# Optimization experiments

Hardware: AMD Instinct MI355X
Metric: run time of the kernel (lower is better)

## Reference

```python
import jax, jax.numpy as jnp
import numpy as np
from jax import lax

EPS = 1e-5

def conv2d(x, w):
    # x: [B,C,H,W], w: [O,I,kh,kw], VALID, stride 1
    return lax.conv_general_dilated(x, w, (1, 1), 'VALID',
                                    dimension_numbers=('NCHW', 'OIHW', 'NCHW'))

def bn_eval(x, g, b, m, v):
    # per-channel eval-mode batchnorm on NCHW
    scale = g / jnp.sqrt(v + EPS)
    return x * scale[None, :, None, None] + (b - m * scale)[None, :, None, None]

def xcorr_depthwise(search, kernel):
    # search: [B,C,Hs,Ws], kernel: [B,C,hk,wk] -> [B,C,Ho,Wo]
    B, C, Hs, Ws = search.shape
    hk, wk = kernel.shape[2], kernel.shape[3]
    s = search.reshape(1, B * C, Hs, Ws)
    k = kernel.reshape(B * C, 1, hk, wk)
    out = lax.conv_general_dilated(s, k, (1, 1), 'VALID',
                                   dimension_numbers=('NCHW', 'OIHW', 'NCHW'),
                                   feature_group_count=B * C)
    return out.reshape(B, C, out.shape[2], out.shape[3])

def setup_inputs() -> dict:
    key = jax.random.key(0)
    ks = jax.random.split(key, 16)
    B, C, HID, OUT = 64, 256, 256, 10
    d = {}
    d['kernel'] = jax.random.normal(ks[0], (B, C, 7, 7), jnp.float32)
    d['search'] = jax.random.normal(ks[1], (B, C, 31, 31), jnp.float32)
    # conv_kernel branch
    d['ck_w'] = jax.random.normal(ks[2], (HID, C, 3, 3), jnp.float32) * 0.02
    d['ck_g'] = jnp.ones((HID,), jnp.float32)
    d['ck_b'] = jnp.zeros((HID,), jnp.float32)
    d['ck_m'] = jax.random.normal(ks[3], (HID,), jnp.float32) * 0.1
    d['ck_v'] = jax.random.uniform(ks[4], (HID,), jnp.float32, 0.5, 1.5)
    # conv_search branch
    d['cs_w'] = jax.random.normal(ks[5], (HID, C, 3, 3), jnp.float32) * 0.02
    d['cs_g'] = jnp.ones((HID,), jnp.float32)
    d['cs_b'] = jnp.zeros((HID,), jnp.float32)
    d['cs_m'] = jax.random.normal(ks[6], (HID,), jnp.float32) * 0.1
    d['cs_v'] = jax.random.uniform(ks[7], (HID,), jnp.float32, 0.5, 1.5)
    # head: 1x1 conv (no bias) + BN + ReLU + 1x1 conv (bias)
    d['h1_w'] = jax.random.normal(ks[8], (HID, HID), jnp.float32) * 0.05
    d['h_g'] = jnp.ones((HID,), jnp.float32)
    d['h_b'] = jnp.zeros((HID,), jnp.float32)
    d['h_m'] = jax.random.normal(ks[9], (HID,), jnp.float32) * 0.1
    d['h_v'] = jax.random.uniform(ks[10], (HID,), jnp.float32, 0.5, 1.5)
    d['h2_w'] = jax.random.normal(ks[11], (OUT, HID), jnp.float32) * 0.05
    d['h2_b'] = jnp.zeros((OUT,), jnp.float32)
    return d

def reference(kernel, search, ck_w, ck_g, ck_b, ck_m, ck_v,
              cs_w, cs_g, cs_b, cs_m, cs_v,
              h1_w, h_g, h_b, h_m, h_v, h2_w, h2_b):
    k = jax.nn.relu(bn_eval(conv2d(kernel, ck_w), ck_g, ck_b, ck_m, ck_v))   # [B,256,5,5]
    s = jax.nn.relu(bn_eval(conv2d(search, cs_w), cs_g, cs_b, cs_m, cs_v))   # [B,256,29,29]
    feat = xcorr_depthwise(s, k)                                             # [B,256,25,25]
    x = jnp.einsum('oi,bihw->bohw', h1_w, feat)
    x = jax.nn.relu(bn_eval(x, h_g, h_b, h_m, h_v))
    out = jnp.einsum('oi,bihw->bohw', h2_w, x) + h2_b[None, :, None, None]   # [B,10,25,25]
    return out
```

## Files before the change

kernel.cpp:

```cpp
#include <hip/hip_runtime.h>
#include <cstddef>
#include <cstdint>

#define BN_EPS 1e-5f

typedef __attribute__((ext_vector_type(8))) __bf16 bf16x8;
typedef __attribute__((ext_vector_type(4))) float f32x4;

__device__ inline unsigned short f2bf(float f) {
    unsigned u = __builtin_bit_cast(unsigned, f);
    unsigned r = (u + 0x7fff + ((u >> 16) & 1)) >> 16;
    return (unsigned short)r;
}
__device__ inline float bf2f(unsigned short u) {
    return __builtin_bit_cast(float, (unsigned)u << 16);
}

#define GLDS16(g, l)                                                        \
    __builtin_amdgcn_global_load_lds(                                       \
        (const __attribute__((address_space(1))) void*)(g),                 \
        (__attribute__((address_space(3))) void*)(l), 16, 0, 0)

template<int H, int W, int WP>
__device__ inline void nhwc_body(int bh, const float* __restrict__ in,
                                 unsigned short* __restrict__ out)
{
    __shared__ unsigned short tl[256][WP];
    const int tid = threadIdx.x;
    const int b = bh / H, h = bh - b * H;
    const int g = tid >> 5, wl = tid & 31;
    const float* base = in + (size_t)b * 256 * (H * W) + (size_t)h * W;
    if (wl < W) {
        #pragma unroll
        for (int cc = 0; cc < 32; ++cc) {
            const int c = cc * 8 + g;
            tl[c][wl] = f2bf(base[(size_t)c * (H * W) + wl]);
        }
    }
    __syncthreads();
    unsigned short* dst = out + (size_t)bh * W * 256 + tid;
    #pragma unroll
    for (int w = 0; w < W; ++w) dst[w * 256] = tl[tid][w];
}

__global__ __launch_bounds__(256)
void prep_kernel(const float* __restrict__ srch, const float* __restrict__ kin,
                 const float* __restrict__ cs_w, const float* __restrict__ ck_w,
                 const float* __restrict__ h1_w, const float* __restrict__ h2_w,
                 unsigned short* __restrict__ s16, unsigned short* __restrict__ k16,
                 unsigned short* __restrict__ wTs, unsigned short* __restrict__ wTk,
                 unsigned short* __restrict__ h1w16, unsigned short* __restrict__ h2w16,
                 int G31, int G7)
{
    const int bid = blockIdx.x;
    if (bid < G31) {
        nhwc_body<31, 31, 33>(bid, srch, s16);
    } else if (bid < G31 + G7) {
        nhwc_body<7, 7, 9>(bid - G31, kin, k16);
    } else {
        const int i = (bid - G31 - G7) * 256 + threadIdx.x;
        if (i < 589824) {
            const int ic = i & 255, t = i >> 8, oc = t & 255, khkw = t >> 8;
            wTs[i] = f2bf(cs_w[(size_t)((oc << 8) + ic) * 9 + khkw]);
        } else if (i < 1179648) {
            const int j = i - 589824;
            const int ic = j & 255, t = j >> 8, oc = t & 255, khkw = t >> 8;
            wTk[j] = f2bf(ck_w[(size_t)((oc << 8) + ic) * 9 + khkw]);
        } else if (i < 1245184) {
            const int j = i - 1179648;
            h1w16[j] = f2bf(h1_w[j]);
        } else if (i < 1249280) {
            const int j = i - 1245184;
            const int oc = j >> 8, ic = j & 255;
            h2w16[j] = (oc < 10) ? f2bf(h2_w[oc * 256 + ic]) : (unsigned short)0;
        }
    }
}

struct ConvParams {
    const unsigned short* bsrc;
    const unsigned short* wT;
    const float *bg, *bb, *bm, *bv;
    unsigned short* out;
    int IH, IW, OW, PPB, N;
};

__global__ __launch_bounds__(256)
void conv3x3_kernel(ConvParams S, ConvParams K, int Gs)
{
    __shared__ __align__(16) unsigned short Alds[128 * 64];
    __shared__ __align__(16) unsigned short Blds[128 * 64];

    const int tid  = threadIdx.x;
    const int lane = tid & 63;
    const int wid  = tid >> 6;

    const int raw = blockIdx.x;
    ConvParams P;
    int tileid;
    if (raw < Gs) {
        P = S;
        const int q8 = Gs >> 3, r8 = Gs & 7;
        const int xcd = raw & 7, seq = raw >> 3;
        tileid = (xcd < r8 ? xcd * (q8 + 1) : r8 * (q8 + 1) + (xcd - r8) * q8) + seq;
    } else {
        P = K;
        tileid = raw - Gs;
    }
    const int pt  = tileid >> 1;
    const int oct = tileid & 1;
    const int oc0 = oct << 7;
    const int p0  = pt << 7;

    int aoff[4], brow[4], bgs8[4], ldsrow[4];
    #pragma unroll
    for (int i = 0; i < 4; ++i) {
        const int r  = i * 32 + wid * 8 + (lane >> 3);
        const int gs = (lane & 7) ^ (r & 7);
        aoff[i] = (oc0 + r) * 256 + gs * 8;
        int pg = p0 + r; if (pg > P.N - 1) pg = P.N - 1;
        const int bb_ = pg / P.PPB;
        const int p   = pg - bb_ * P.PPB;
        const int oh  = p / P.OW, ow = p - oh * P.OW;
        brow[i] = (bb_ * P.IH + oh) * P.IW + ow;
        bgs8[i] = gs * 8;
        ldsrow[i] = (i * 32 + wid * 8) * 64;
    }

    const int q_  = lane >> 4;
    const int lr  = lane & 15;
    const int wm0 = (wid >> 1) * 64;
    const int wn0 = (wid & 1) * 64;
    const int g0  = q_ ^ (lane & 7);
    const int g1  = (4 + q_) ^ (lane & 7);
    const unsigned short* Abase = &Alds[(wm0 + lr) * 64];
    const unsigned short* Bbase = &Blds[(wn0 + lr) * 64];

    f32x4 acc[4][4] = {};

    int kh = 0, kw = 0;
    for (int khkw = 0; khkw < 9; ++khkw) {
        const size_t wslice = (size_t)khkw << 16;
        const int tapadd = kh * P.IW + kw;
        for (int ics = 0; ics < 4; ++ics) {
            const int ic0 = ics * 64;
            __syncthreads();
            #pragma unroll
            for (int i = 0; i < 4; ++i) {
                GLDS16(P.wT + wslice + aoff[i] + ic0, &Alds[ldsrow[i]]);
                GLDS16(P.bsrc + (size_t)(brow[i] + tapadd) * 256 + ic0 + bgs8[i],
                       &Blds[ldsrow[i]]);
            }
            __syncthreads();

            bf16x8 bfr[4][2];
            #pragma unroll
            for (int n = 0; n < 4; ++n) {
                bfr[n][0] = *(const bf16x8*)(Bbase + n * 1024 + g0 * 8);
                bfr[n][1] = *(const bf16x8*)(Bbase + n * 1024 + g1 * 8);
            }
            #pragma unroll
            for (int m = 0; m < 4; ++m) {
                bf16x8 a0 = *(const bf16x8*)(Abase + m * 1024 + g0 * 8);
                bf16x8 a1 = *(const bf16x8*)(Abase + m * 1024 + g1 * 8);
                #pragma unroll
                for (int n = 0; n < 4; ++n) {
                    acc[m][n] = __builtin_amdgcn_mfma_f32_16x16x32_bf16(
                                    a0, bfr[n][0], acc[m][n], 0, 0, 0);
                    acc[m][n] = __builtin_amdgcn_mfma_f32_16x16x32_bf16(
                                    a1, bfr[n][1], acc[m][n], 0, 0, 0);
                }
            }
        }
        if (++kw == 3) { kw = 0; ++kh; }
    }

    #pragma unroll
    for (int m = 0; m < 4; ++m) {
        const int ocm = oc0 + wm0 + m * 16 + q_ * 4;
        float sc[4], sh[4];
        #pragma unroll
        for (int r = 0; r < 4; ++r) {
            sc[r] = P.bg[ocm + r] * rsqrtf(P.bv[ocm + r] + BN_EPS);
            sh[r] = P.bb[ocm + r] - P.bm[ocm + r] * sc[r];
        }
        #pragma unroll
        for (int n = 0; n < 4; ++n) {
            const int pg = p0 + wn0 + n * 16 + lr;
            if (pg < P.N) {
                unsigned e0 = f2bf(fmaxf(acc[m][n][0] * sc[0] + sh[0], 0.f));
                unsigned e1 = f2bf(fmaxf(acc[m][n][1] * sc[1] + sh[1], 0.f));
                unsigned e2 = f2bf(fmaxf(acc[m][n][2] * sc[2] + sh[2], 0.f));
                unsigned e3 = f2bf(fmaxf(acc[m][n][3] * sc[3] + sh[3], 0.f));
                uint2 v; v.x = e0 | (e1 << 16); v.y = e2 | (e3 << 16);
                *(uint2*)(P.out + (size_t)pg * 256 + ocm) = v;
            }
        }
    }
}

__global__ __launch_bounds__(256)
void xcorr_nhwc_kernel(const unsigned short* __restrict__ sfeat,
                       const unsigned short* __restrict__ kfeat,
                       unsigned short* __restrict__ xc2)
{
    const int bid = blockIdx.x;
    const int b = bid / 25, oh = bid - b * 25;
    const int c = threadIdx.x;

    float kv[25];
    const unsigned short* kp = kfeat + (size_t)b * 25 * 256 + c;
    #pragma unroll
    for (int t = 0; t < 25; ++t) kv[t] = bf2f(kp[t * 256]);

    float acc[25];
    #pragma unroll
    for (int ow = 0; ow < 25; ++ow) acc[ow] = 0.f;

    const unsigned short* sp = sfeat + ((size_t)(b * 29 + oh)) * 29 * 256 + c;
    #pragma unroll
    for (int i = 0; i < 5; ++i) {
        #pragma unroll
        for (int w = 0; w < 29; ++w) {
            const float sv = bf2f(sp[(i * 29 + w) * 256]);
            #pragma unroll
            for (int j = 0; j < 5; ++j) {
                if (j <= w && w - j <= 24)
                    acc[w - j] += sv * kv[i * 5 + j];
            }
        }
    }

    unsigned short* op = xc2 + ((size_t)(b * 625 + oh * 25)) * 256 + c;
    #pragma unroll
    for (int ow = 0; ow < 25; ++ow) op[ow * 256] = f2bf(acc[ow]);
}

__global__ __launch_bounds__(256)
void fused_head_kernel(const unsigned short* __restrict__ xc2,
                       const unsigned short* __restrict__ h1w16,
                       const unsigned short* __restrict__ h2w16,
                       const float* __restrict__ bn_g,
                       const float* __restrict__ bn_b,
                       const float* __restrict__ bn_m,
                       const float* __restrict__ bn_v,
                       const float* __restrict__ h2b,
                       float* __restrict__ out)
{
    __shared__ __align__(16) unsigned short lds[20480];
    unsigned short* Alds = lds;
    unsigned short* Blds = lds + 16384;
    unsigned short* Ylds = lds;

    const int tid  = threadIdx.x;
    const int lane = tid & 63;
    const int wid  = tid >> 6;
    const int p0   = blockIdx.x * 64;

    const int lrow = lane >> 3;
    const int gs   = 0;
    (void)gs;

    int aoffs[8], aldsr[8];
    #pragma unroll
    for (int s = 0; s < 8; ++s) {
        const int rowb = s * 32 + wid * 8;
        const int row  = rowb + lrow;
        const int g    = (lane & 7) ^ (row & 7);
        aoffs[s] = row * 256 + g * 8;
        aldsr[s] = rowb * 64;
    }
    int boffs[2], bldsr[2];
    #pragma unroll
    for (int t = 0; t < 2; ++t) {
        const int rowb = t * 32 + wid * 8;
        const int row  = rowb + lrow;
        const int g    = (lane & 7) ^ (row & 7);
        boffs[t] = (p0 + row) * 256 + g * 8;
        bldsr[t] = rowb * 64;
    }

    const int q_ = lane >> 4;
    const int lr = lane & 15;
    const int wm = wid >> 1;
    const int wn = wid & 1;
    const int g0 = q_ ^ (lane & 7);
    const int g1 = (4 + q_) ^ (lane & 7);
    const unsigned short* Abase = &Alds[(wm * 128 + lr) * 64];
    const unsigned short* Bbase = &Blds[(wn * 32 + lr) * 64];

    f32x4 acc[8][2] = {};

    for (int ics = 0; ics < 4; ++ics) {
        const int ic0 = ics * 64;
        __syncthreads();
        #pragma unroll
        for (int s = 0; s < 8; ++s)
            GLDS16(h1w16 + aoffs[s] + ic0, &Alds[aldsr[s]]);
        #pragma unroll
        for (int t = 0; t < 2; ++t)
            GLDS16(xc2 + boffs[t] + ic0, &Blds[bldsr[t]]);
        __syncthreads();

        bf16x8 bfr[2][2];
        #pragma unroll
        for (int n = 0; n < 2; ++n) {
            bfr[n][0] = *(const bf16x8*)(Bbase + n * 1024 + g0 * 8);
            bfr[n][1] = *(const bf16x8*)(Bbase + n * 1024 + g1 * 8);
        }
        #pragma unroll
        for (int m = 0; m < 8; ++m) {
            bf16x8 a0 = *(const bf16x8*)(Abase + m * 1024 + g0 * 8);
            bf16x8 a1 = *(const bf16x8*)(Abase + m * 1024 + g1 * 8);
            #pragma unroll
            for (int n = 0; n < 2; ++n) {
                acc[m][n] = __builtin_amdgcn_mfma_f32_16x16x32_bf16(
                                a0, bfr[n][0], acc[m][n], 0, 0, 0);
                acc[m][n] = __builtin_amdgcn_mfma_f32_16x16x32_bf16(
                                a1, bfr[n][1], acc[m][n], 0, 0, 0);
            }
        }
    }

    __syncthreads();
    #pragma unroll
    for (int m = 0; m < 8; ++m) {
        const int ocm = wm * 128 + m * 16 + q_ * 4;
        float sc[4], sh[4];
        #pragma unroll
        for (int r = 0; r < 4; ++r) {
            sc[r] = bn_g[ocm + r] * rsqrtf(bn_v[ocm + r] + BN_EPS);
            sh[r] = bn_b[ocm + r] - bn_m[ocm + r] * sc[r];
        }
        #pragma unroll
        for (int n = 0; n < 2; ++n) {
            const int pl = wn * 32 + n * 16 + lr;
            unsigned e0 = f2bf(fmaxf(acc[m][n][0] * sc[0] + sh[0], 0.f));
            unsigned e1 = f2bf(fmaxf(acc[m][n][1] * sc[1] + sh[1], 0.f));
            unsigned e2 = f2bf(fmaxf(acc[m][n][2] * sc[2] + sh[2], 0.f));
            unsigned e3 = f2bf(fmaxf(acc[m][n][3] * sc[3] + sh[3], 0.f));
            uint2 v; v.x = e0 | (e1 << 16); v.y = e2 | (e3 << 16);
            *(uint2*)(Ylds + (size_t)pl * 264 + ocm) = v;
        }
    }
    __syncthreads();

    const int pl = wid * 16 + lr;
    const unsigned short* arow = h2w16 + lr * 256 + q_ * 8;
    const unsigned short* brow = Ylds + (size_t)pl * 264 + q_ * 8;

    f32x4 acc2 = {};
    #pragma unroll
    for (int ks = 0; ks < 8; ++ks) {
        bf16x8 a  = *(const bf16x8*)(arow + ks * 32);
        bf16x8 bb = *(const bf16x8*)(brow + ks * 32);
        acc2 = __builtin_amdgcn_mfma_f32_16x16x32_bf16(a, bb, acc2, 0, 0, 0);
    }

    const int pg = p0 + pl;
    const int b = pg / 625, p = pg - b * 625;
    #pragma unroll
    for (int r = 0; r < 4; ++r) {
        const int oc = q_ * 4 + r;
        if (oc < 10)
            out[((size_t)(b * 10 + oc)) * 625 + p] = acc2[r] + h2b[oc];
    }
}

extern "C" void kernel_launch(void* const* d_in, const int* in_sizes, int n_in,
                              void* d_out, int out_size, void* d_ws, size_t ws_size,
                              hipStream_t stream)
{
    const float* kin  = (const float*)d_in[0];
    const float* srch = (const float*)d_in[1];
    const float* ck_w = (const float*)d_in[2];
    const float* ck_g = (const float*)d_in[3];
    const float* ck_b = (const float*)d_in[4];
    const float* ck_m = (const float*)d_in[5];
    const float* ck_v = (const float*)d_in[6];
    const float* cs_w = (const float*)d_in[7];
    const float* cs_g = (const float*)d_in[8];
    const float* cs_b = (const float*)d_in[9];
    const float* cs_m = (const float*)d_in[10];
    const float* cs_v = (const float*)d_in[11];
    const float* h1_w = (const float*)d_in[12];
    const float* h_g  = (const float*)d_in[13];
    const float* h_b  = (const float*)d_in[14];
    const float* h_m  = (const float*)d_in[15];
    const float* h_v  = (const float*)d_in[16];
    const float* h2_w = (const float*)d_in[17];
    const float* h2_b = (const float*)d_in[18];

    const int B = in_sizes[0] / (256 * 7 * 7);

    uint8_t* w = (uint8_t*)d_ws;
    unsigned short* s16     = (unsigned short*)(w);
    unsigned short* xc2     = (unsigned short*)(w);
    unsigned short* sfeat16 = (unsigned short*)(w + 31490048);
    unsigned short* kf16    = (unsigned short*)(w + 59047936);
    unsigned short* k16     = (unsigned short*)(w + 59867136);
    unsigned short* wTk     = (unsigned short*)(w + 61472768);
    unsigned short* wTs     = (unsigned short*)(w + 62652416);
    unsigned short* h1w16   = (unsigned short*)(w + 63832064);
    unsigned short* h2w16   = (unsigned short*)(w + 63963136);

    const int Ns = B * 841;
    const int Nk = B * 25;
    const int Nh = B * 625;
    const int Gs = 2 * ((Ns + 127) / 128);
    const int Gk = 2 * ((Nk + 127) / 128);
    const int G31 = B * 31, G7 = B * 7;

    dim3 blk(256, 1, 1);

    hipLaunchKernelGGL(prep_kernel, dim3(G31 + G7 + 4880), blk, 0, stream,
                       srch, kin, cs_w, ck_w, h1_w, h2_w,
                       s16, k16, wTs, wTk, h1w16, h2w16, G31, G7);

    ConvParams S{ s16, wTs, cs_g, cs_b, cs_m, cs_v, sfeat16, 31, 31, 29, 841, Ns };
    ConvParams K{ k16, wTk, ck_g, ck_b, ck_m, ck_v, kf16, 7, 7, 5, 25, Nk };
    hipLaunchKernelGGL(conv3x3_kernel, dim3(Gs + Gk), blk, 0, stream, S, K, Gs);

    hipLaunchKernelGGL(xcorr_nhwc_kernel, dim3(B * 25), blk, 0, stream,
                       sfeat16, kf16, xc2);

    hipLaunchKernelGGL(fused_head_kernel, dim3(Nh / 64), blk, 0, stream,
                       xc2, h1w16, h2w16, h_g, h_b, h_m, h_v, h2_b,
                       (float*)d_out);
}
```

Before: 166.6 us.

## Fuse depthwise xcorr into head GEMM kernel and retile input transposes

The depthwise cross-correlation is now computed inside the head kernel, with each block producing 64 output pixels of one batch directly into shared memory. This removes the intermediate xc2 global buffer and one kernel launch. Blocks now tile per batch (10 per image, the last one padded with zeros). The NCHW-to-NHWC input transpose is also reworked into 64x64 channel-by-pixel tiles for better coalescing. The cost is redundant xcorr work, since overlapping output rows are recomputed across block boundaries, and some waste in the padded tail tile.

New measurement: 165.3 us. About the same (-0.8%).

```diff
diff --git a/kernel.cpp b/kernel.cpp
--- a/kernel.cpp
+++ b/kernel.cpp
@@ -21,26 +21,32 @@
         (const __attribute__((address_space(1))) void*)(g),                 \
         (__attribute__((address_space(3))) void*)(l), 16, 0, 0)
 
-template<int H, int W, int WP>
-__device__ inline void nhwc_body(int bh, const float* __restrict__ in,
-                                 unsigned short* __restrict__ out)
+template<int HW, int HWT>
+__device__ inline void transpose_body(int rb, const float* __restrict__ in,
+                                      unsigned short* __restrict__ out)
 {
-    __shared__ unsigned short tl[256][WP];
-    const int tid = threadIdx.x;
-    const int b = bh / H, h = bh - b * H;
-    const int g = tid >> 5, wl = tid & 31;
-    const float* base = in + (size_t)b * 256 * (H * W) + (size_t)h * W;
-    if (wl < W) {
-        #pragma unroll
-        for (int cc = 0; cc < 32; ++cc) {
-            const int c = cc * 8 + g;
-            tl[c][wl] = f2bf(base[(size_t)c * (H * W) + wl]);
-        }
+    __shared__ unsigned short tl[64][66];
+    const int tid  = threadIdx.x;
+    const int lane = tid & 63, w = tid >> 6;
+    const int b  = rb / (HWT * 4);
+    const int r2 = rb - b * (HWT * 4);
+    const int ht = r2 >> 2, ct = r2 & 3;
+    const int c0 = ct * 64, hw0 = ht * 64;
+    const int hw = hw0 + lane;
+    const float* ib = in + ((size_t)b * 256 + c0) * HW;
+    #pragma unroll
+    for (int r = 0; r < 16; ++r) {
+        const int cl = w * 16 + r;
+        const float v = (hw < HW) ? ib[(size_t)cl * HW + hw] : 0.f;
+        tl[cl][lane] = f2bf(v);
     }
     __syncthreads();
-    unsigned short* dst = out + (size_t)bh * W * 256 + tid;
-    #pragma unroll
-    for (int w = 0; w < W; ++w) dst[w * 256] = tl[tid][w];
+    unsigned short* ob = out + ((size_t)b * HW + hw0) * 256 + c0 + lane;
+    #pragma unroll
+    for (int jj = 0; jj < 16; ++jj) {
+        const int j = jj * 4 + w;
+        if (hw0 + j < HW) ob[(size_t)j * 256] = tl[lane][j];
+    }
 }
 
 __global__ __launch_bounds__(256)
@@ -50,15 +56,15 @@
                  unsigned short* __restrict__ s16, unsigned short* __restrict__ k16,
                  unsigned short* __restrict__ wTs, unsigned short* __restrict__ wTk,
                  unsigned short* __restrict__ h1w16, unsigned short* __restrict__ h2w16,
-                 int G31, int G7)
+                 int GS, int GK)
 {
     const int bid = blockIdx.x;
-    if (bid < G31) {
-        nhwc_body<31, 31, 33>(bid, srch, s16);
-    } else if (bid < G31 + G7) {
-        nhwc_body<7, 7, 9>(bid - G31, kin, k16);
+    if (bid < GS) {
+        transpose_body<961, 16>(bid, srch, s16);
+    } else if (bid < GS + GK) {
+        transpose_body<49, 1>(bid - GS, kin, k16);
     } else {
-        const int i = (bid - G31 - G7) * 256 + threadIdx.x;
+        const int i = (bid - GS - GK) * 256 + threadIdx.x;
         if (i < 589824) {
             const int ic = i & 255, t = i >> 8, oc = t & 255, khkw = t >> 8;
             wTs[i] = f2bf(cs_w[(size_t)((oc << 8) + ic) * 9 + khkw]);
@@ -200,67 +206,73 @@
 }
 
 __global__ __launch_bounds__(256)
-void xcorr_nhwc_kernel(const unsigned short* __restrict__ sfeat,
-                       const unsigned short* __restrict__ kfeat,
-                       unsigned short* __restrict__ xc2)
+void fused_xcorr_head_kernel(const unsigned short* __restrict__ sfeat,
+                             const unsigned short* __restrict__ kfeat,
+                             const unsigned short* __restrict__ h1w16,
+                             const unsigned short* __restrict__ h2w16,
+                             const float* __restrict__ bn_g,
+                             const float* __restrict__ bn_b,
+                             const float* __restrict__ bn_m,
+                             const float* __restrict__ bn_v,
+                             const float* __restrict__ h2b,
+                             float* __restrict__ out)
 {
-    const int bid = blockIdx.x;
-    const int b = bid / 25, oh = bid - b * 25;
-    const int c = threadIdx.x;
-
-    float kv[25];
-    const unsigned short* kp = kfeat + (size_t)b * 25 * 256 + c;
-    #pragma unroll
-    for (int t = 0; t < 25; ++t) kv[t] = bf2f(kp[t * 256]);
-
-    float acc[25];
-    #pragma unroll
-    for (int ow = 0; ow < 25; ++ow) acc[ow] = 0.f;
-
-    const unsigned short* sp = sfeat + ((size_t)(b * 29 + oh)) * 29 * 256 + c;
-    #pragma unroll
-    for (int i = 0; i < 5; ++i) {
-        #pragma unroll
-        for (int w = 0; w < 29; ++w) {
-            const float sv = bf2f(sp[(i * 29 + w) * 256]);
-            #pragma unroll
-            for (int j = 0; j < 5; ++j) {
-                if (j <= w && w - j <= 24)
-                    acc[w - j] += sv * kv[i * 5 + j];
-            }
-        }
-    }
-
-    unsigned short* op = xc2 + ((size_t)(b * 625 + oh * 25)) * 256 + c;
-    #pragma unroll
-    for (int ow = 0; ow < 25; ++ow) op[ow * 256] = f2bf(acc[ow]);
-}
-
-__global__ __launch_bounds__(256)
-void fused_head_kernel(const unsigned short* __restrict__ xc2,
-                       const unsigned short* __restrict__ h1w16,
-                       const unsigned short* __restrict__ h2w16,
-                       const float* __restrict__ bn_g,
-                       const float* __restrict__ bn_b,
-                       const float* __restrict__ bn_m,
-                       const float* __restrict__ bn_v,
-                       const float* __restrict__ h2b,
-                       float* __restrict__ out)
-{
-    __shared__ __align__(16) unsigned short lds[20480];
-    unsigned short* Alds = lds;
-    unsigned short* Blds = lds + 16384;
-    unsigned short* Ylds = lds;
+    __shared__ __align__(16) unsigned short Alds[16384];
+    __shared__ __align__(16) unsigned short Xlds[64 * 264];
 
     const int tid  = threadIdx.x;
     const int lane = tid & 63;
     const int wid  = tid >> 6;
-    const int p0   = blockIdx.x * 64;
+    const int bid  = blockIdx.x;
+    const int b    = bid / 10;
+    const int pt   = bid - b * 10;
+    const int p0   = pt * 64;
+
+    {
+        const int c = tid;
+        float kv[25];
+        const unsigned short* kp = kfeat + (size_t)b * 25 * 256 + c;
+        #pragma unroll
+        for (int t = 0; t < 25; ++t) kv[t] = bf2f(kp[t * 256]);
+
+        if (pt == 9) {
+            #pragma unroll
+            for (int j = 49; j < 64; ++j) Xlds[j * 264 + c] = 0;
+        }
+
+        const int oh0 = p0 / 25;
+        for (int ohr = 0; ohr < 4; ++ohr) {
+            const int oh = oh0 + ohr;
+            const int jbase = oh * 25 - p0;
+            if (oh <= 24 && jbase < 64) {
+                float acc[25];
+                #pragma unroll
+                for (int z = 0; z < 25; ++z) acc[z] = 0.f;
+                const unsigned short* sp =
+                    sfeat + ((size_t)(b * 29 + oh)) * 29 * 256 + c;
+                #pragma unroll
+                for (int i = 0; i < 5; ++i)
+                    #pragma unroll
+                    for (int w2 = 0; w2 < 29; ++w2) {
+                        const float sv = bf2f(sp[(i * 29 + w2) * 256]);
+                        #pragma unroll
+                        for (int t = 0; t < 5; ++t) {
+                            const int ww = w2 - t;
+                            if (ww >= 0 && ww <= 24)
+                                acc[ww] += sv * kv[i * 5 + t];
+                        }
+                    }
+                #pragma unroll
+                for (int ow = 0; ow < 25; ++ow) {
+                    const int j = jbase + ow;
+                    if (j >= 0 && j < 64)
+                        Xlds[j * 264 + c] = f2bf(acc[ow]);
+                }
+            }
+        }
+    }
 
     const int lrow = lane >> 3;
-    const int gs   = 0;
-    (void)gs;
-
     int aoffs[8], aldsr[8];
     #pragma unroll
     for (int s = 0; s < 8; ++s) {
@@ -270,16 +282,6 @@
         aoffs[s] = row * 256 + g * 8;
         aldsr[s] = rowb * 64;
     }
-    int boffs[2], bldsr[2];
-    #pragma unroll
-    for (int t = 0; t < 2; ++t) {
-        const int rowb = t * 32 + wid * 8;
-        const int row  = rowb + lrow;
-        const int g    = (lane & 7) ^ (row & 7);
-        boffs[t] = (p0 + row) * 256 + g * 8;
-        bldsr[t] = rowb * 64;
-    }
-
     const int q_ = lane >> 4;
     const int lr = lane & 15;
     const int wm = wid >> 1;
@@ -287,9 +289,8 @@
     const int g0 = q_ ^ (lane & 7);
     const int g1 = (4 + q_) ^ (lane & 7);
     const unsigned short* Abase = &Alds[(wm * 128 + lr) * 64];
-    const unsigned short* Bbase = &Blds[(wn * 32 + lr) * 64];
-
-    f32x4 acc[8][2] = {};
+
+    f32x4 acc1[8][2] = {};
 
     for (int ics = 0; ics < 4; ++ics) {
         const int ic0 = ics * 64;
@@ -297,16 +298,14 @@
         #pragma unroll
         for (int s = 0; s < 8; ++s)
             GLDS16(h1w16 + aoffs[s] + ic0, &Alds[aldsr[s]]);
-        #pragma unroll
-        for (int t = 0; t < 2; ++t)
-            GLDS16(xc2 + boffs[t] + ic0, &Blds[bldsr[t]]);
         __syncthreads();
 
         bf16x8 bfr[2][2];
         #pragma unroll
         for (int n = 0; n < 2; ++n) {
-            bfr[n][0] = *(const bf16x8*)(Bbase + n * 1024 + g0 * 8);
-            bfr[n][1] = *(const bf16x8*)(Bbase + n * 1024 + g1 * 8);
+            const int rowp = wn * 32 + n * 16 + lr;
+            bfr[n][0] = *(const bf16x8*)(Xlds + rowp * 264 + ic0 + q_ * 8);
+            bfr[n][1] = *(const bf16x8*)(Xlds + rowp * 264 + ic0 + 32 + q_ * 8);
         }
         #pragma unroll
         for (int m = 0; m < 8; ++m) {
@@ -314,10 +313,10 @@
             bf16x8 a1 = *(const bf16x8*)(Abase + m * 1024 + g1 * 8);
             #pragma unroll
             for (int n = 0; n < 2; ++n) {
-                acc[m][n] = __builtin_amdgcn_mfma_f32_16x16x32_bf16(
-                                a0, bfr[n][0], acc[m][n], 0, 0, 0);
-                acc[m][n] = __builtin_amdgcn_mfma_f32_16x16x32_bf16(
-                                a1, bfr[n][1], acc[m][n], 0, 0, 0);
+                acc1[m][n] = __builtin_amdgcn_mfma_f32_16x16x32_bf16(
+                                 a0, bfr[n][0], acc1[m][n], 0, 0, 0);
+                acc1[m][n] = __builtin_amdgcn_mfma_f32_16x16x32_bf16(
+                                 a1, bfr[n][1], acc1[m][n], 0, 0, 0);
             }
         }
     }
@@ -335,19 +334,19 @@
         #pragma unroll
         for (int n = 0; n < 2; ++n) {
             const int pl = wn * 32 + n * 16 + lr;
-            unsigned e0 = f2bf(fmaxf(acc[m][n][0] * sc[0] + sh[0], 0.f));
-            unsigned e1 = f2bf(fmaxf(acc[m][n][1] * sc[1] + sh[1], 0.f));
-            unsigned e2 = f2bf(fmaxf(acc[m][n][2] * sc[2] + sh[2], 0.f));
-            unsigned e3 = f2bf(fmaxf(acc[m][n][3] * sc[3] + sh[3], 0.f));
+            unsigned e0 = f2bf(fmaxf(acc1[m][n][0] * sc[0] + sh[0], 0.f));
+            unsigned e1 = f2bf(fmaxf(acc1[m][n][1] * sc[1] + sh[1], 0.f));
+            unsigned e2 = f2bf(fmaxf(acc1[m][n][2] * sc[2] + sh[2], 0.f));
+            unsigned e3 = f2bf(fmaxf(acc1[m][n][3] * sc[3] + sh[3], 0.f));
             uint2 v; v.x = e0 | (e1 << 16); v.y = e2 | (e3 << 16);
-            *(uint2*)(Ylds + (size_t)pl * 264 + ocm) = v;
+            *(uint2*)(Xlds + (size_t)pl * 264 + ocm) = v;
         }
     }
     __syncthreads();
 
     const int pl = wid * 16 + lr;
     const unsigned short* arow = h2w16 + lr * 256 + q_ * 8;
-    const unsigned short* brow = Ylds + (size_t)pl * 264 + q_ * 8;
+    const unsigned short* brow = Xlds + (size_t)pl * 264 + q_ * 8;
 
     f32x4 acc2 = {};
     #pragma unroll
@@ -357,13 +356,14 @@
         acc2 = __builtin_amdgcn_mfma_f32_16x16x32_bf16(a, bb, acc2, 0, 0, 0);
     }
 
-    const int pg = p0 + pl;
-    const int b = pg / 625, p = pg - b * 625;
-    #pragma unroll
-    for (int r = 0; r < 4; ++r) {
-        const int oc = q_ * 4 + r;
-        if (oc < 10)
-            out[((size_t)(b * 10 + oc)) * 625 + p] = acc2[r] + h2b[oc];
+    const int plocal = p0 + pl;
+    if (plocal < 625) {
+        #pragma unroll
+        for (int r = 0; r < 4; ++r) {
+            const int oc = q_ * 4 + r;
+            if (oc < 10)
+                out[((size_t)(b * 10 + oc)) * 625 + plocal] = acc2[r] + h2b[oc];
+        }
     }
 }
 
@@ -395,7 +395,6 @@
 
     uint8_t* w = (uint8_t*)d_ws;
     unsigned short* s16     = (unsigned short*)(w);
-    unsigned short* xc2     = (unsigned short*)(w);
     unsigned short* sfeat16 = (unsigned short*)(w + 31490048);
     unsigned short* kf16    = (unsigned short*)(w + 59047936);
     unsigned short* k16     = (unsigned short*)(w + 59867136);
@@ -406,25 +405,22 @@
 
     const int Ns = B * 841;
     const int Nk = B * 25;
-    const int Nh = B * 625;
     const int Gs = 2 * ((Ns + 127) / 128);
     const int Gk = 2 * ((Nk + 127) / 128);
-    const int G31 = B * 31, G7 = B * 7;
+    const int GS = B * 16 * 4;
+    const int GK = B * 1 * 4;
 
     dim3 blk(256, 1, 1);
 
-    hipLaunchKernelGGL(prep_kernel, dim3(G31 + G7 + 4880), blk, 0, stream,
+    hipLaunchKernelGGL(prep_kernel, dim3(GS + GK + 4880), blk, 0, stream,
                        srch, kin, cs_w, ck_w, h1_w, h2_w,
-                       s16, k16, wTs, wTk, h1w16, h2w16, G31, G7);
+                       s16, k16, wTs, wTk, h1w16, h2w16, GS, GK);
 
     ConvParams S{ s16, wTs, cs_g, cs_b, cs_m, cs_v, sfeat16, 31, 31, 29, 841, Ns };
     ConvParams K{ k16, wTk, ck_g, ck_b, ck_m, ck_v, kf16, 7, 7, 5, 25, Nk };
     hipLaunchKernelGGL(conv3x3_kernel, dim3(Gs + Gk), blk, 0, stream, S, K, Gs);
 
-    hipLaunchKernelGGL(xcorr_nhwc_kernel, dim3(B * 25), blk, 0, stream,
-                       sfeat16, kf16, xc2);
-
-    hipLaunchKernelGGL(fused_head_kernel, dim3(Nh / 64), blk, 0, stream,
-                       xc2, h1w16, h2w16, h_g, h_b, h_m, h_v, h2_b,
-                       (float*)d_out);
-}
+    hipLaunchKernelGGL(fused_xcorr_head_kernel, dim3(B * 10), blk, 0, stream,
+                       sfeat16, kf16, h1w16, h2w16,
+                       h_g, h_b, h_m, h_v, h2_b, (float*)d_out);
+}
```
